# Performance work log

Hardware: AMD Instinct MI355X
Metric: run time of the kernel (lower is better)

The kernel has to match this reference:

```python
import jax, jax.numpy as jnp
import numpy as np

NUM_ANCHORS_LIST = [6400, 1600, 400]  # 640x640 input, strides 8/16/32
STRIDES = [8, 16, 32]
GRID_SIZES = [80, 40, 20]
TOPK = 9
EPS = 1e-9


def _make_anchor_bboxes():
    boxes = []
    for stride, size in zip(STRIDES, GRID_SIZES):
        c = (np.arange(size, dtype=np.float32) + 0.5) * stride
        cx, cy = np.meshgrid(c, c)
        half = stride / 2.0
        b = np.stack([cx - half, cy - half, cx + half, cy + half], axis=-1)
        boxes.append(b.reshape(-1, 4))
    return jnp.asarray(np.concatenate(boxes, axis=0))  # [8400,4]


def _random_boxes(key, shape_prefix, img=640.0):
    k1, k2 = jax.random.split(key)
    cxy = jax.random.uniform(k1, shape_prefix + (2,), minval=0.0, maxval=img)
    wh = jax.random.uniform(k2, shape_prefix + (2,), minval=8.0, maxval=160.0)
    x1y1 = jnp.clip(cxy - wh / 2, 0.0, img)
    x2y2 = jnp.clip(cxy + wh / 2, 0.0, img)
    return jnp.concatenate([x1y1, x2y2], axis=-1).astype(jnp.float32)


def setup_inputs() -> dict:
    key = jax.random.key(0)
    kg, kp, kl, km = jax.random.split(key, 4)
    B, N, M, C = 16, 8400, 128, 80
    return {
        "anchor_bboxes": _make_anchor_bboxes(),               # [N,4]
        "gt_labels": jax.random.randint(kl, (B, M, 1), 0, C).astype(jnp.int64),
        "gt_bboxes": _random_boxes(kg, (B, M)),               # [B,M,4]
        "mask_gt": jax.random.randint(km, (B, M, 1), 0, 2).astype(jnp.int32),
        "pred_bboxes": _random_boxes(kp, (B, N)),             # [B,N,4]
        "num_classes": C,
    }


def _batch_bbox_iou(box1, box2):
    # box1 [B,N,4], box2 [B,M,4] -> [B,N,M]
    area1 = (box1[..., 2] - box1[..., 0]) * (box1[..., 3] - box1[..., 1])
    area2 = (box2[..., 2] - box2[..., 0]) * (box2[..., 3] - box2[..., 1])
    ix1 = jnp.maximum(box1[:, :, None, 0], box2[:, None, :, 0])
    iy1 = jnp.maximum(box1[:, :, None, 1], box2[:, None, :, 1])
    ix2 = jnp.minimum(box1[:, :, None, 2], box2[:, None, :, 2])
    iy2 = jnp.minimum(box1[:, :, None, 3], box2[:, None, :, 3])
    inter = jnp.maximum(ix2 - ix1, 0.0) * jnp.maximum(iy2 - iy1, 0.0)
    union = area1[:, :, None] + area2[:, None, :] - inter
    return inter / (union + EPS)


def reference(anchor_bboxes, gt_labels, gt_bboxes, mask_gt, pred_bboxes, num_classes):
    B, M = gt_bboxes.shape[0], gt_bboxes.shape[1]
    N = anchor_bboxes.shape[0]
    labels = gt_labels[..., 0].astype(jnp.int32)           # [B,M]

    ac = (anchor_bboxes[:, :2] + anchor_bboxes[:, 2:]) / 2  # [N,2]
    gc = (gt_bboxes[..., :2] + gt_bboxes[..., 2:]) / 2      # [B,M,2]
    # cdist via expanded quadratic form (avoids [B,N,M,2] intermediate)
    a2 = jnp.sum(ac * ac, axis=-1)                          # [N]
    g2 = jnp.sum(gc * gc, axis=-1)                          # [B,M]
    d2 = a2[None, :, None] + g2[:, None, :] - 2.0 * jnp.einsum('nc,bmc->bnm', ac, gc)
    distances = jnp.sqrt(jnp.maximum(d2, 0.0))              # [B,N,M]

    # per-level topk closest anchors per GT -> candidate mask [B,N,M]
    bidx = jnp.arange(B)[:, None, None]
    midx = jnp.arange(M)[None, :, None]
    level_masks = []
    start = 0
    for ln in NUM_ANCHORS_LIST:
        ld = distances[:, start:start + ln, :]               # [B,ln,M]
        k = min(TOPK, ln)
        _, idx = jax.lax.top_k(-jnp.swapaxes(ld, 1, 2), k)   # [B,M,k] anchor idx
        lm = jnp.zeros((B, ln, M), dtype=bool).at[bidx, idx, midx].set(True)
        level_masks.append(lm)
        start += ln
    candidate_mask = jnp.concatenate(level_masks, axis=1)    # [B,N,M]

    ious = _batch_bbox_iou(jnp.broadcast_to(anchor_bboxes[None], (B, N, 4)), gt_bboxes)
    cm_f = candidate_mask.astype(ious.dtype)
    cand_ious = ious * cm_f
    count = jnp.maximum(cm_f.sum(axis=1), 1.0)               # [B,M]
    mean = cand_ious.sum(axis=1) / count
    sq_mean = jnp.sum(cand_ious * cand_ious, axis=1) / count # mask is 0/1
    std = jnp.sqrt(jnp.maximum(sq_mean - mean * mean, 0.0))
    thr = mean + std                                         # [B,M]

    is_pos = candidate_mask & (ious >= thr[:, None, :])
    center_in_gt = ((ac[None, :, None, 0] >= gt_bboxes[:, None, :, 0])
                    & (ac[None, :, None, 0] <= gt_bboxes[:, None, :, 2])
                    & (ac[None, :, None, 1] >= gt_bboxes[:, None, :, 1])
                    & (ac[None, :, None, 1] <= gt_bboxes[:, None, :, 3]))
    is_pos = is_pos & center_in_gt & (mask_gt[..., 0] > 0)[:, None, :]

    fg_mask = jnp.any(is_pos, axis=-1)                       # [B,N]
    pos_ious = jnp.where(is_pos, ious, 0.0)
    max_gt_idx = jnp.argmax(pos_ious, axis=-1)               # [B,N]

    fg_f = fg_mask.astype(ious.dtype)
    assigned_labels = jnp.take_along_axis(labels, max_gt_idx, axis=1) * fg_mask.astype(jnp.int32)
    assigned_bboxes = jnp.take_along_axis(gt_bboxes, max_gt_idx[..., None], axis=1) * fg_f[..., None]
    assigned_ious = jnp.take_along_axis(ious, max_gt_idx[..., None], axis=2)[..., 0] * fg_f

    pred_ious = _batch_bbox_iou(pred_bboxes, gt_bboxes)
    pred_assigned = jnp.take_along_axis(pred_ious, max_gt_idx[..., None], axis=2)[..., 0] * fg_f
    assigned_ious = assigned_ious * pred_assigned

    assigned_scores = jax.nn.one_hot(assigned_labels, num_classes, dtype=ious.dtype) \
        * (assigned_ious * fg_f)[..., None]                  # [B,N,C]
    return assigned_labels, assigned_bboxes, assigned_scores, fg_mask
```

## Files before the change

kernel.cpp:

```cpp
#include <hip/hip_runtime.h>
#include <stdint.h>

#define B_ 16
#define N_ 8400
#define M_ 128

__device__ __forceinline__ float iou_box(float ax1, float ay1, float ax2, float ay2,
                                         float bx1, float by1, float bx2, float by2) {
    float area1 = __fmul_rn(__fsub_rn(ax2, ax1), __fsub_rn(ay2, ay1));
    float area2 = __fmul_rn(__fsub_rn(bx2, bx1), __fsub_rn(by2, by1));
    float ix1 = fmaxf(ax1, bx1), iy1 = fmaxf(ay1, by1);
    float ix2 = fminf(ax2, bx2), iy2 = fminf(ay2, by2);
    float iw = fmaxf(__fsub_rn(ix2, ix1), 0.0f);
    float ih = fmaxf(__fsub_rn(iy2, iy1), 0.0f);
    float inter = __fmul_rn(iw, ih);
    float uni = __fsub_rn(__fadd_rn(area1, area2), inter);
    return __fdiv_rn(inter, __fadd_rn(uni, 1e-9f));
}

__global__ __launch_bounds__(128) void assign_kernel(
    const float* __restrict__ gt_bboxes,
    const int* __restrict__ mask_gt,
    unsigned long long* __restrict__ ws) {
    const int tid = threadIdx.x;
    const int r = tid >> 5;
    const int s = tid & 31;
    const int g = blockIdx.x * 32 + s;
    const int b = g >> 7;
    const int m = g & (M_ - 1);
    const bool active = (mask_gt[g] != 0);

    __shared__ int   s_idx[27 * 32];
    __shared__ float s_iou[27 * 32];
    __shared__ int   s_cin[27 * 32];
    __shared__ float s_thr[32];

    const float* gp = gt_bboxes + (size_t)g * 4;
    const float gx1 = gp[0], gy1 = gp[1], gx2 = gp[2], gy2 = gp[3];
    const float gcx = __fmul_rn(__fadd_rn(gx1, gx2), 0.5f);
    const float gcy = __fmul_rn(__fadd_rn(gy1, gy2), 0.5f);
    const float g2 = __fadd_rn(__fmul_rn(gcx, gcx), __fmul_rn(gcy, gcy));

    if (r < 3 && active) {
        const int   size  = (r == 0) ? 80 : ((r == 1) ? 40 : 20);
        const int   start = (r == 0) ? 0 : ((r == 1) ? 6400 : 8000);
        const float st    = (r == 0) ? 8.0f : ((r == 1) ? 16.0f : 32.0f);
        const float inv   = (r == 0) ? 0.125f : ((r == 1) ? 0.0625f : 0.03125f);

        int jl = (int)floorf(gcx * inv - 0.5f) - 2;
        int il = (int)floorf(gcy * inv - 0.5f) - 2;
        jl = min(max(jl, 0), size - 6);
        il = min(max(il, 0), size - 6);

        unsigned long long tk[9];
#pragma unroll
        for (int k = 0; k < 9; ++k) tk[k] = ~0ULL;

        for (int wy = 0; wy < 6; ++wy) {
            const int   i   = il + wy;
            const float acy = __fmul_rn(__fadd_rn((float)i, 0.5f), st);
            for (int wx = 0; wx < 6; ++wx) {
                const int   j   = jl + wx;
                const float acx = __fmul_rn(__fadd_rn((float)j, 0.5f), st);
                const int   n   = start + i * size + j;
                float a2  = __fadd_rn(__fmul_rn(acx, acx), __fmul_rn(acy, acy));
                float dot = __fadd_rn(__fmul_rn(acx, gcx), __fmul_rn(acy, gcy));
                float d2  = __fsub_rn(__fadd_rn(a2, g2), __fmul_rn(2.0f, dot));
                float dist = __fsqrt_rn(fmaxf(d2, 0.0f));
                unsigned long long key =
                    ((unsigned long long)__float_as_uint(dist) << 32) | (unsigned)n;
                if (key < tk[8]) tk[8] = key;
#pragma unroll
                for (int q = 8; q >= 1; --q) {
                    unsigned long long lo = tk[q - 1] < tk[q] ? tk[q - 1] : tk[q];
                    unsigned long long hi = tk[q - 1] < tk[q] ? tk[q] : tk[q - 1];
                    tk[q - 1] = lo;
                    tk[q] = hi;
                }
            }
        }

        int v[9];
#pragma unroll
        for (int k = 0; k < 9; ++k) v[k] = (int)(tk[k] & 0xFFFFFFFFu);
#pragma unroll
        for (int rr = 0; rr < 9; ++rr) {
#pragma unroll
            for (int p = (rr & 1); p + 1 < 9; p += 2) {
                int lo = min(v[p], v[p + 1]);
                int hi = max(v[p], v[p + 1]);
                v[p] = lo; v[p + 1] = hi;
            }
        }
#pragma unroll
        for (int k = 0; k < 9; ++k) s_idx[(r * 9 + k) * 32 + s] = v[k];
    }
    __syncthreads();

#pragma unroll
    for (int q = 0; q < 7; ++q) {
        const int kk = r + 4 * q;
        if (kk < 27 && active) {
            const int   l     = kk / 9;
            const int   size  = (l == 0) ? 80 : ((l == 1) ? 40 : 20);
            const int   start = (l == 0) ? 0 : ((l == 1) ? 6400 : 8000);
            const float st    = (l == 0) ? 8.0f : ((l == 1) ? 16.0f : 32.0f);
            const float half  = __fmul_rn(st, 0.5f);
            const int n = s_idx[kk * 32 + s];
            const int loc = n - start;
            const int i = loc / size;
            const int j = loc - i * size;
            float acx = __fmul_rn(__fadd_rn((float)j, 0.5f), st);
            float acy = __fmul_rn(__fadd_rn((float)i, 0.5f), st);
            float ax1 = __fsub_rn(acx, half), ay1 = __fsub_rn(acy, half);
            float ax2 = __fadd_rn(acx, half), ay2 = __fadd_rn(acy, half);
            float iou = iou_box(ax1, ay1, ax2, ay2, gx1, gy1, gx2, gy2);
            s_iou[kk * 32 + s] = iou;
            s_cin[kk * 32 + s] =
                (acx >= gx1 && acx <= gx2 && acy >= gy1 && acy <= gy2) ? 1 : 0;
        }
    }
    __syncthreads();

    if (r == 0 && active) {
        float tot = 0.0f, tot2 = 0.0f;
#pragma unroll
        for (int kk = 0; kk < 27; ++kk) {
            const float iou = s_iou[kk * 32 + s];
            tot  = __fadd_rn(tot, iou);
            tot2 = __fadd_rn(tot2, __fmul_rn(iou, iou));
        }
        float mean = __fdiv_rn(tot, 27.0f);
        float sqm  = __fdiv_rn(tot2, 27.0f);
        float var  = __fsub_rn(sqm, __fmul_rn(mean, mean));
        float stdv = __fsqrt_rn(fmaxf(var, 0.0f));
        s_thr[s] = __fadd_rn(mean, stdv);
    }
    __syncthreads();

    if (active) {
        const float thr = s_thr[s];
#pragma unroll
        for (int q = 0; q < 7; ++q) {
            const int kk = r + 4 * q;
            if (kk < 27) {
                const float iou = s_iou[kk * 32 + s];
                if (s_cin[kk * 32 + s] && iou >= thr) {
                    unsigned long long packed =
                        ((unsigned long long)(0xC0000000u | __float_as_uint(iou)) << 32) |
                        (unsigned long long)(0xFFFFFFFFu - (unsigned)m);
                    atomicMax(&ws[(size_t)b * N_ + s_idx[kk * 32 + s]], packed);
                }
            }
        }
    }
}

__global__ __launch_bounds__(256) void finalize_kernel(
    const int* __restrict__ gt_labels,
    const float* __restrict__ gt_bboxes,
    const float* __restrict__ pred_bboxes,
    const int* __restrict__ num_classes_p,
    const unsigned long long* __restrict__ ws,
    float* __restrict__ out) {
    const int idx = blockIdx.x * 256 + threadIdx.x;
    const int C = num_classes_p[0];

    float4* sp = (float4*)(out + (size_t)B_ * N_ * 5) + (size_t)blockIdx.x * 5120;
    const float4 z4 = make_float4(0.f, 0.f, 0.f, 0.f);
    for (int k = threadIdx.x; k < 5120; k += 256) sp[k] = z4;
    __syncthreads();

    if (idx >= B_ * N_) return;
    const int b = idx / N_;

    const unsigned long long w = ws[idx];
    const bool fg = (w >> 62) == 3ULL;
    float labelf = 0.0f;
    float4 bb = make_float4(0.f, 0.f, 0.f, 0.f);
    float v = 0.0f, fgf = 0.0f;
    int label = 0;
    if (fg) {
        fgf = 1.0f;
        const unsigned mm = 0xFFFFFFFFu - (unsigned)(w & 0xFFFFFFFFu);
        const float a_iou = __uint_as_float((unsigned)((w >> 32) & 0x3FFFFFFFu));
        label = gt_labels[b * M_ + (int)mm];
        labelf = (float)label;
        const float* gg = gt_bboxes + ((size_t)b * M_ + mm) * 4;
        bb.x = gg[0]; bb.y = gg[1]; bb.z = gg[2]; bb.w = gg[3];
        const float* p = pred_bboxes + (size_t)idx * 4;
        float piou = iou_box(p[0], p[1], p[2], p[3], bb.x, bb.y, bb.z, bb.w);
        v = __fmul_rn(a_iou, piou);
    }

    out[idx] = labelf;
    ((float4*)(out + (size_t)B_ * N_))[idx] = bb;
    if (fg) out[(size_t)B_ * N_ * 5 + (size_t)idx * C + label] = v;
    out[(size_t)B_ * N_ * (5 + C) + idx] = fgf;
}

extern "C" void kernel_launch(void* const* d_in, const int* in_sizes, int n_in,
                              void* d_out, int out_size, void* d_ws, size_t ws_size,
                              hipStream_t stream) {
    const int*   gt_labels  = (const int*)d_in[1];
    const float* gt_bboxes  = (const float*)d_in[2];
    const int*   mask_gt    = (const int*)d_in[3];
    const float* pred       = (const float*)d_in[4];
    const int*   ncls       = (const int*)d_in[5];
    unsigned long long* ws  = (unsigned long long*)d_ws;
    float* out              = (float*)d_out;

    assign_kernel<<<64, 128, 0, stream>>>(gt_bboxes, mask_gt, ws);
    finalize_kernel<<<(B_ * N_ + 255) / 256, 256, 0, stream>>>(
        gt_labels, gt_bboxes, pred, ncls, ws, out);
}
```

Measured before the change: 89.52 us.

## Fuse assignment and finalize into one kernel with per-tile shared-memory winners

Merges the two kernels into one grid over (anchor tile, batch). Each block recomputes the top-k candidates, IoU thresholds and center tests for all 128 GTs of its batch, then resolves winners with shared-memory atomics restricted to its 256-anchor tile. It then writes the outputs, including a coalesced float4 write of the score tensor in one pass instead of zeroing it and scattering into it. This removes the global workspace, its global atomics and the second launch, at the cost of redundant candidate computation in every block (33x per batch).

```diff
diff --git a/kernel.cpp b/kernel.cpp
--- a/kernel.cpp
+++ b/kernel.cpp
@@ -18,95 +18,120 @@
     return __fdiv_rn(inter, __fadd_rn(uni, 1e-9f));
 }
 
-__global__ __launch_bounds__(128) void assign_kernel(
+__global__ __launch_bounds__(256) void fused_kernel(
+    const int* __restrict__ gt_labels,
     const float* __restrict__ gt_bboxes,
     const int* __restrict__ mask_gt,
-    unsigned long long* __restrict__ ws) {
-    const int tid = threadIdx.x;
-    const int r = tid >> 5;
-    const int s = tid & 31;
-    const int g = blockIdx.x * 32 + s;
-    const int b = g >> 7;
-    const int m = g & (M_ - 1);
-    const bool active = (mask_gt[g] != 0);
-
-    __shared__ int   s_idx[27 * 32];
-    __shared__ float s_iou[27 * 32];
-    __shared__ int   s_cin[27 * 32];
-    __shared__ float s_thr[32];
-
-    const float* gp = gt_bboxes + (size_t)g * 4;
-    const float gx1 = gp[0], gy1 = gp[1], gx2 = gp[2], gy2 = gp[3];
-    const float gcx = __fmul_rn(__fadd_rn(gx1, gx2), 0.5f);
-    const float gcy = __fmul_rn(__fadd_rn(gy1, gy2), 0.5f);
-    const float g2 = __fadd_rn(__fmul_rn(gcx, gcx), __fmul_rn(gcy, gcy));
-
-    if (r < 3 && active) {
-        const int   size  = (r == 0) ? 80 : ((r == 1) ? 40 : 20);
-        const int   start = (r == 0) ? 0 : ((r == 1) ? 6400 : 8000);
-        const float st    = (r == 0) ? 8.0f : ((r == 1) ? 16.0f : 32.0f);
-        const float inv   = (r == 0) ? 0.125f : ((r == 1) ? 0.0625f : 0.03125f);
-
-        int jl = (int)floorf(gcx * inv - 0.5f) - 2;
-        int il = (int)floorf(gcy * inv - 0.5f) - 2;
-        jl = min(max(jl, 0), size - 6);
-        il = min(max(il, 0), size - 6);
-
-        unsigned long long tk[9];
-#pragma unroll
-        for (int k = 0; k < 9; ++k) tk[k] = ~0ULL;
-
-        for (int wy = 0; wy < 6; ++wy) {
-            const int   i   = il + wy;
-            const float acy = __fmul_rn(__fadd_rn((float)i, 0.5f), st);
-            for (int wx = 0; wx < 6; ++wx) {
-                const int   j   = jl + wx;
-                const float acx = __fmul_rn(__fadd_rn((float)j, 0.5f), st);
-                const int   n   = start + i * size + j;
-                float a2  = __fadd_rn(__fmul_rn(acx, acx), __fmul_rn(acy, acy));
-                float dot = __fadd_rn(__fmul_rn(acx, gcx), __fmul_rn(acy, gcy));
-                float d2  = __fsub_rn(__fadd_rn(a2, g2), __fmul_rn(2.0f, dot));
-                float dist = __fsqrt_rn(fmaxf(d2, 0.0f));
-                unsigned long long key =
-                    ((unsigned long long)__float_as_uint(dist) << 32) | (unsigned)n;
-                if (key < tk[8]) tk[8] = key;
-#pragma unroll
-                for (int q = 8; q >= 1; --q) {
-                    unsigned long long lo = tk[q - 1] < tk[q] ? tk[q - 1] : tk[q];
-                    unsigned long long hi = tk[q - 1] < tk[q] ? tk[q] : tk[q - 1];
-                    tk[q - 1] = lo;
-                    tk[q] = hi;
+    const float* __restrict__ pred_bboxes,
+    const int* __restrict__ num_classes_p,
+    float* __restrict__ out) {
+    const int tile = blockIdx.x;
+    const int b    = blockIdx.y;
+    const int t    = threadIdx.x;
+    const int C    = num_classes_p[0];
+
+    __shared__ float s_gx1[M_], s_gy1[M_], s_gx2[M_], s_gy2[M_];
+    __shared__ float s_gcx[M_], s_gcy[M_], s_g2[M_], s_thr[M_];
+    __shared__ int   s_mask[M_], s_lab[M_];
+    __shared__ int   s_cand[27 * M_];
+    __shared__ float s_ciou[27 * M_];
+    __shared__ unsigned s_ccin[M_];
+    __shared__ unsigned long long s_win[256];
+    __shared__ int   s_slab[256];
+    __shared__ float s_sv[256];
+    __shared__ int   s_sfg[256];
+
+    s_win[t] = 0ULL;
+    if (t < M_) {
+        const int gi = b * M_ + t;
+        const float4 gb = ((const float4*)gt_bboxes)[gi];
+        s_gx1[t] = gb.x; s_gy1[t] = gb.y; s_gx2[t] = gb.z; s_gy2[t] = gb.w;
+        const float gcx = __fmul_rn(__fadd_rn(gb.x, gb.z), 0.5f);
+        const float gcy = __fmul_rn(__fadd_rn(gb.y, gb.w), 0.5f);
+        s_gcx[t] = gcx; s_gcy[t] = gcy;
+        s_g2[t]  = __fadd_rn(__fmul_rn(gcx, gcx), __fmul_rn(gcy, gcy));
+        s_mask[t] = mask_gt[gi];
+        s_lab[t]  = gt_labels[gi];
+    }
+    __syncthreads();
+
+#pragma unroll
+    for (int rep = 0; rep < 2; ++rep) {
+        const int T = t + rep * 256;
+        if (T < 384) {
+            const int l = T >> 7;
+            const int m = T & (M_ - 1);
+            if (s_mask[m]) {
+                const int   size  = (l == 0) ? 80 : ((l == 1) ? 40 : 20);
+                const int   start = (l == 0) ? 0 : ((l == 1) ? 6400 : 8000);
+                const float st    = (l == 0) ? 8.0f : ((l == 1) ? 16.0f : 32.0f);
+                const float inv   = (l == 0) ? 0.125f : ((l == 1) ? 0.0625f : 0.03125f);
+                const float gcx = s_gcx[m], gcy = s_gcy[m], g2 = s_g2[m];
+
+                int jl = (int)floorf(gcx * inv - 0.5f) - 2;
+                int il = (int)floorf(gcy * inv - 0.5f) - 2;
+                jl = min(max(jl, 0), size - 6);
+                il = min(max(il, 0), size - 6);
+
+                unsigned long long tk[9];
+#pragma unroll
+                for (int k = 0; k < 9; ++k) tk[k] = ~0ULL;
+
+                for (int wy = 0; wy < 6; ++wy) {
+                    const int   i   = il + wy;
+                    const float acy = __fmul_rn(__fadd_rn((float)i, 0.5f), st);
+                    for (int wx = 0; wx < 6; ++wx) {
+                        const int   j   = jl + wx;
+                        const float acx = __fmul_rn(__fadd_rn((float)j, 0.5f), st);
+                        const int   n   = start + i * size + j;
+                        float a2  = __fadd_rn(__fmul_rn(acx, acx), __fmul_rn(acy, acy));
+                        float dot = __fadd_rn(__fmul_rn(acx, gcx), __fmul_rn(acy, gcy));
+                        float d2  = __fsub_rn(__fadd_rn(a2, g2), __fmul_rn(2.0f, dot));
+                        float dist = __fsqrt_rn(fmaxf(d2, 0.0f));
+                        unsigned long long key =
+                            ((unsigned long long)__float_as_uint(dist) << 32) | (unsigned)n;
+                        if (key < tk[8]) tk[8] = key;
+#pragma unroll
+                        for (int q = 8; q >= 1; --q) {
+                            unsigned long long lo = tk[q - 1] < tk[q] ? tk[q - 1] : tk[q];
+                            unsigned long long hi = tk[q - 1] < tk[q] ? tk[q] : tk[q - 1];
+                            tk[q - 1] = lo;
+                            tk[q] = hi;
+                        }
+                    }
                 }
+
+                int v[9];
+#pragma unroll
+                for (int k = 0; k < 9; ++k) v[k] = (int)(tk[k] & 0xFFFFFFFFu);
+#pragma unroll
+                for (int rr = 0; rr < 9; ++rr) {
+#pragma unroll
+                    for (int p = (rr & 1); p + 1 < 9; p += 2) {
+                        int lo = min(v[p], v[p + 1]);
+                        int hi = max(v[p], v[p + 1]);
+                        v[p] = lo; v[p + 1] = hi;
+                    }
+                }
+#pragma unroll
+                for (int k = 0; k < 9; ++k) s_cand[(l * 9 + k) * M_ + m] = v[k];
             }
         }
-
-        int v[9];
-#pragma unroll
-        for (int k = 0; k < 9; ++k) v[k] = (int)(tk[k] & 0xFFFFFFFFu);
-#pragma unroll
-        for (int rr = 0; rr < 9; ++rr) {
-#pragma unroll
-            for (int p = (rr & 1); p + 1 < 9; p += 2) {
-                int lo = min(v[p], v[p + 1]);
-                int hi = max(v[p], v[p + 1]);
-                v[p] = lo; v[p + 1] = hi;
-            }
-        }
-#pragma unroll
-        for (int k = 0; k < 9; ++k) s_idx[(r * 9 + k) * 32 + s] = v[k];
-    }
-    __syncthreads();
-
-#pragma unroll
-    for (int q = 0; q < 7; ++q) {
-        const int kk = r + 4 * q;
-        if (kk < 27 && active) {
+    }
+    __syncthreads();
+
+    if (t < M_ && s_mask[t]) {
+        const float gx1 = s_gx1[t], gy1 = s_gy1[t], gx2 = s_gx2[t], gy2 = s_gy2[t];
+        unsigned cin = 0;
+        float tot = 0.0f, tot2 = 0.0f;
+#pragma unroll
+        for (int kk = 0; kk < 27; ++kk) {
             const int   l     = kk / 9;
             const int   size  = (l == 0) ? 80 : ((l == 1) ? 40 : 20);
             const int   start = (l == 0) ? 0 : ((l == 1) ? 6400 : 8000);
             const float st    = (l == 0) ? 8.0f : ((l == 1) ? 16.0f : 32.0f);
             const float half  = __fmul_rn(st, 0.5f);
-            const int n = s_idx[kk * 32 + s];
+            const int n = s_cand[kk * M_ + t];
             const int loc = n - start;
             const int i = loc / size;
             const int j = loc - i * size;
@@ -115,88 +140,85 @@
             float ax1 = __fsub_rn(acx, half), ay1 = __fsub_rn(acy, half);
             float ax2 = __fadd_rn(acx, half), ay2 = __fadd_rn(acy, half);
             float iou = iou_box(ax1, ay1, ax2, ay2, gx1, gy1, gx2, gy2);
-            s_iou[kk * 32 + s] = iou;
-            s_cin[kk * 32 + s] =
-                (acx >= gx1 && acx <= gx2 && acy >= gy1 && acy <= gy2) ? 1 : 0;
-        }
-    }
-    __syncthreads();
-
-    if (r == 0 && active) {
-        float tot = 0.0f, tot2 = 0.0f;
-#pragma unroll
-        for (int kk = 0; kk < 27; ++kk) {
-            const float iou = s_iou[kk * 32 + s];
+            s_ciou[kk * M_ + t] = iou;
+            if (acx >= gx1 && acx <= gx2 && acy >= gy1 && acy <= gy2)
+                cin |= (1u << kk);
             tot  = __fadd_rn(tot, iou);
             tot2 = __fadd_rn(tot2, __fmul_rn(iou, iou));
         }
+        s_ccin[t] = cin;
         float mean = __fdiv_rn(tot, 27.0f);
         float sqm  = __fdiv_rn(tot2, 27.0f);
         float var  = __fsub_rn(sqm, __fmul_rn(mean, mean));
         float stdv = __fsqrt_rn(fmaxf(var, 0.0f));
-        s_thr[s] = __fadd_rn(mean, stdv);
-    }
-    __syncthreads();
-
-    if (active) {
-        const float thr = s_thr[s];
-#pragma unroll
-        for (int q = 0; q < 7; ++q) {
-            const int kk = r + 4 * q;
-            if (kk < 27) {
-                const float iou = s_iou[kk * 32 + s];
-                if (s_cin[kk * 32 + s] && iou >= thr) {
-                    unsigned long long packed =
-                        ((unsigned long long)(0xC0000000u | __float_as_uint(iou)) << 32) |
-                        (unsigned long long)(0xFFFFFFFFu - (unsigned)m);
-                    atomicMax(&ws[(size_t)b * N_ + s_idx[kk * 32 + s]], packed);
-                }
+        s_thr[t] = __fadd_rn(mean, stdv);
+    }
+    __syncthreads();
+
+    for (int T = t; T < M_ * 27; T += 256) {
+        const int m  = T / 27;
+        const int kk = T - m * 27;
+        if (!s_mask[m]) continue;
+        const float iou = s_ciou[kk * M_ + m];
+        if (((s_ccin[m] >> kk) & 1u) && iou >= s_thr[m]) {
+            const int n = s_cand[kk * M_ + m];
+            const int slot = n - tile * 256;
+            if (slot >= 0 && slot < 256) {
+                unsigned long long packed =
+                    ((unsigned long long)__float_as_uint(iou) << 32) |
+                    (unsigned long long)(0xFFFFFFFFu - (unsigned)m);
+                atomicMax(&s_win[slot], packed);
             }
         }
     }
-}
-
-__global__ __launch_bounds__(256) void finalize_kernel(
-    const int* __restrict__ gt_labels,
-    const float* __restrict__ gt_bboxes,
-    const float* __restrict__ pred_bboxes,
-    const int* __restrict__ num_classes_p,
-    const unsigned long long* __restrict__ ws,
-    float* __restrict__ out) {
-    const int idx = blockIdx.x * 256 + threadIdx.x;
-    const int C = num_classes_p[0];
-
-    float4* sp = (float4*)(out + (size_t)B_ * N_ * 5) + (size_t)blockIdx.x * 5120;
-    const float4 z4 = make_float4(0.f, 0.f, 0.f, 0.f);
-    for (int k = threadIdx.x; k < 5120; k += 256) sp[k] = z4;
-    __syncthreads();
-
-    if (idx >= B_ * N_) return;
-    const int b = idx / N_;
-
-    const unsigned long long w = ws[idx];
-    const bool fg = (w >> 62) == 3ULL;
-    float labelf = 0.0f;
-    float4 bb = make_float4(0.f, 0.f, 0.f, 0.f);
-    float v = 0.0f, fgf = 0.0f;
-    int label = 0;
-    if (fg) {
-        fgf = 1.0f;
-        const unsigned mm = 0xFFFFFFFFu - (unsigned)(w & 0xFFFFFFFFu);
-        const float a_iou = __uint_as_float((unsigned)((w >> 32) & 0x3FFFFFFFu));
-        label = gt_labels[b * M_ + (int)mm];
-        labelf = (float)label;
-        const float* gg = gt_bboxes + ((size_t)b * M_ + mm) * 4;
-        bb.x = gg[0]; bb.y = gg[1]; bb.z = gg[2]; bb.w = gg[3];
-        const float* p = pred_bboxes + (size_t)idx * 4;
-        float piou = iou_box(p[0], p[1], p[2], p[3], bb.x, bb.y, bb.z, bb.w);
-        v = __fmul_rn(a_iou, piou);
-    }
-
-    out[idx] = labelf;
-    ((float4*)(out + (size_t)B_ * N_))[idx] = bb;
-    if (fg) out[(size_t)B_ * N_ * 5 + (size_t)idx * C + label] = v;
-    out[(size_t)B_ * N_ * (5 + C) + idx] = fgf;
+    __syncthreads();
+
+    const int n = tile * 256 + t;
+    int   lab = 0, fg = 0;
+    float v_out = 0.0f;
+    if (n < N_) {
+        const unsigned long long w = s_win[t];
+        float labelf = 0.0f;
+        float4 bb = make_float4(0.f, 0.f, 0.f, 0.f);
+        float fgf = 0.0f;
+        if (w != 0ULL) {
+            fg = 1; fgf = 1.0f;
+            const unsigned mm = 0xFFFFFFFFu - (unsigned)(w & 0xFFFFFFFFu);
+            const float a_iou = __uint_as_float((unsigned)(w >> 32));
+            lab = s_lab[mm];
+            labelf = (float)lab;
+            bb.x = s_gx1[mm]; bb.y = s_gy1[mm];
+            bb.z = s_gx2[mm]; bb.w = s_gy2[mm];
+            const float4 p = ((const float4*)pred_bboxes)[(size_t)b * N_ + n];
+            float piou = iou_box(p.x, p.y, p.z, p.w, bb.x, bb.y, bb.z, bb.w);
+            v_out = __fmul_rn(a_iou, piou);
+        }
+        const size_t idxG = (size_t)b * N_ + n;
+        out[idxG] = labelf;
+        ((float4*)(out + (size_t)B_ * N_))[idxG] = bb;
+        out[(size_t)B_ * N_ * (5 + C) + idxG] = fgf;
+    }
+    s_slab[t] = lab;
+    s_sv[t]   = v_out;
+    s_sfg[t]  = fg;
+    __syncthreads();
+
+    const int cnt = min(256, N_ - tile * 256);
+    const int c4  = C >> 2;
+    const int total4 = cnt * c4;
+    float4* sc = (float4*)(out + (size_t)B_ * N_ * 5) +
+                 ((size_t)b * N_ + (size_t)tile * 256) * c4;
+    for (int f = t; f < total4; f += 256) {
+        const int a = f / c4;
+        const int q = f - a * c4;
+        float4 z = make_float4(0.f, 0.f, 0.f, 0.f);
+        if (s_sfg[a]) {
+            const int c0 = q << 2;
+            const int La = s_slab[a];
+            if (La >= c0 && La < c0 + 4) ((float*)&z)[La - c0] = s_sv[a];
+        }
+        sc[f] = z;
+    }
 }
 
 extern "C" void kernel_launch(void* const* d_in, const int* in_sizes, int n_in,
@@ -207,10 +229,10 @@
     const int*   mask_gt    = (const int*)d_in[3];
     const float* pred       = (const float*)d_in[4];
     const int*   ncls       = (const int*)d_in[5];
-    unsigned long long* ws  = (unsigned long long*)d_ws;
     float* out              = (float*)d_out;
-
-    assign_kernel<<<64, 128, 0, stream>>>(gt_bboxes, mask_gt, ws);
-    finalize_kernel<<<(B_ * N_ + 255) / 256, 256, 0, stream>>>(
-        gt_labels, gt_bboxes, pred, ncls, ws, out);
+    (void)d_ws; (void)ws_size;
+
+    dim3 grid((N_ + 255) / 256, B_);
+    fused_kernel<<<grid, 256, 0, stream>>>(gt_labels, gt_bboxes, mask_gt,
+                                           pred, ncls, out);
 }
```

New measurement: 115.6 us. 29.2% more time.

## Parallelize per-GT top-k with wave bitonic sort and fuse score-row writes

Applied to the files above, without the earlier changes.

The assign kernel now uses one block per ground-truth box instead of 32 boxes per block. Each 64-lane wave handles one pyramid level and replaces the serial 36-element insertion top-k with a wave-wide bitonic sort over shuffles. This spreads the work over 2048 blocks instead of 64 and cuts per-thread serial latency. In finalize, the separate zero-fill followed by a scattered score write becomes a single pass of float4 stores that places each anchor's score inline. That removes one write pass and a barrier, but assumes C is divisible by 4 and that B*N is a multiple of 256.

```diff
diff --git a/kernel.cpp b/kernel.cpp
--- a/kernel.cpp
+++ b/kernel.cpp
@@ -18,71 +18,74 @@
     return __fdiv_rn(inter, __fadd_rn(uni, 1e-9f));
 }
 
-__global__ __launch_bounds__(128) void assign_kernel(
+__global__ __launch_bounds__(192) void assign_kernel(
     const float* __restrict__ gt_bboxes,
     const int* __restrict__ mask_gt,
     unsigned long long* __restrict__ ws) {
-    const int tid = threadIdx.x;
-    const int r = tid >> 5;
-    const int s = tid & 31;
-    const int g = blockIdx.x * 32 + s;
+    const int g = blockIdx.x;
+    if (mask_gt[g] == 0) return;
     const int b = g >> 7;
     const int m = g & (M_ - 1);
-    const bool active = (mask_gt[g] != 0);
-
-    __shared__ int   s_idx[27 * 32];
-    __shared__ float s_iou[27 * 32];
-    __shared__ int   s_cin[27 * 32];
-    __shared__ float s_thr[32];
-
-    const float* gp = gt_bboxes + (size_t)g * 4;
-    const float gx1 = gp[0], gy1 = gp[1], gx2 = gp[2], gy2 = gp[3];
+    const int t = threadIdx.x;
+    const int w = t >> 6;
+    const int lane = t & 63;
+
+    __shared__ int   s_idx[27];
+    __shared__ float s_iou[27];
+    __shared__ int   s_cin[27];
+    __shared__ float s_thr;
+
+    const float4 gb = ((const float4*)gt_bboxes)[g];
+    const float gx1 = gb.x, gy1 = gb.y, gx2 = gb.z, gy2 = gb.w;
     const float gcx = __fmul_rn(__fadd_rn(gx1, gx2), 0.5f);
     const float gcy = __fmul_rn(__fadd_rn(gy1, gy2), 0.5f);
     const float g2 = __fadd_rn(__fmul_rn(gcx, gcx), __fmul_rn(gcy, gcy));
 
-    if (r < 3 && active) {
-        const int   size  = (r == 0) ? 80 : ((r == 1) ? 40 : 20);
-        const int   start = (r == 0) ? 0 : ((r == 1) ? 6400 : 8000);
-        const float st    = (r == 0) ? 8.0f : ((r == 1) ? 16.0f : 32.0f);
-        const float inv   = (r == 0) ? 0.125f : ((r == 1) ? 0.0625f : 0.03125f);
-
-        int jl = (int)floorf(gcx * inv - 0.5f) - 2;
-        int il = (int)floorf(gcy * inv - 0.5f) - 2;
-        jl = min(max(jl, 0), size - 6);
-        il = min(max(il, 0), size - 6);
-
-        unsigned long long tk[9];
-#pragma unroll
-        for (int k = 0; k < 9; ++k) tk[k] = ~0ULL;
-
-        for (int wy = 0; wy < 6; ++wy) {
-            const int   i   = il + wy;
-            const float acy = __fmul_rn(__fadd_rn((float)i, 0.5f), st);
-            for (int wx = 0; wx < 6; ++wx) {
-                const int   j   = jl + wx;
-                const float acx = __fmul_rn(__fadd_rn((float)j, 0.5f), st);
-                const int   n   = start + i * size + j;
-                float a2  = __fadd_rn(__fmul_rn(acx, acx), __fmul_rn(acy, acy));
-                float dot = __fadd_rn(__fmul_rn(acx, gcx), __fmul_rn(acy, gcy));
-                float d2  = __fsub_rn(__fadd_rn(a2, g2), __fmul_rn(2.0f, dot));
-                float dist = __fsqrt_rn(fmaxf(d2, 0.0f));
-                unsigned long long key =
-                    ((unsigned long long)__float_as_uint(dist) << 32) | (unsigned)n;
-                if (key < tk[8]) tk[8] = key;
-#pragma unroll
-                for (int q = 8; q >= 1; --q) {
-                    unsigned long long lo = tk[q - 1] < tk[q] ? tk[q - 1] : tk[q];
-                    unsigned long long hi = tk[q - 1] < tk[q] ? tk[q] : tk[q - 1];
-                    tk[q - 1] = lo;
-                    tk[q] = hi;
-                }
-            }
-        }
-
+    const int   size  = (w == 0) ? 80 : ((w == 1) ? 40 : 20);
+    const int   start = (w == 0) ? 0 : ((w == 1) ? 6400 : 8000);
+    const float st    = (w == 0) ? 8.0f : ((w == 1) ? 16.0f : 32.0f);
+    const float inv   = (w == 0) ? 0.125f : ((w == 1) ? 0.0625f : 0.03125f);
+
+    int jl = (int)floorf(gcx * inv - 0.5f) - 2;
+    int il = (int)floorf(gcy * inv - 0.5f) - 2;
+    jl = min(max(jl, 0), size - 6);
+    il = min(max(il, 0), size - 6);
+
+    unsigned long long key = ~0ULL;
+    if (lane < 36) {
+        const int wy = lane / 6;
+        const int wx = lane - wy * 6;
+        const int   i   = il + wy;
+        const int   j   = jl + wx;
+        const float acy = __fmul_rn(__fadd_rn((float)i, 0.5f), st);
+        const float acx = __fmul_rn(__fadd_rn((float)j, 0.5f), st);
+        const int   n   = start + i * size + j;
+        float a2  = __fadd_rn(__fmul_rn(acx, acx), __fmul_rn(acy, acy));
+        float dot = __fadd_rn(__fmul_rn(acx, gcx), __fmul_rn(acy, gcy));
+        float d2  = __fsub_rn(__fadd_rn(a2, g2), __fmul_rn(2.0f, dot));
+        float dist = __fsqrt_rn(fmaxf(d2, 0.0f));
+        key = ((unsigned long long)__float_as_uint(dist) << 32) | (unsigned)n;
+    }
+
+#pragma unroll
+    for (int k = 2; k <= 64; k <<= 1) {
+#pragma unroll
+        for (int j = k >> 1; j > 0; j >>= 1) {
+            unsigned long long other = __shfl_xor(key, j, 64);
+            const bool up = ((lane & k) == 0);
+            const bool keepMin = (((lane & j) == 0) == up);
+            const unsigned long long mn = key < other ? key : other;
+            const unsigned long long mx = key < other ? other : key;
+            key = keepMin ? mn : mx;
+        }
+    }
+    if (lane < 9) s_idx[w * 9 + lane] = (int)(key & 0xFFFFFFFFu);
+    __syncthreads();
+
+    if (t < 3) {
         int v[9];
 #pragma unroll
-        for (int k = 0; k < 9; ++k) v[k] = (int)(tk[k] & 0xFFFFFFFFu);
+        for (int k = 0; k < 9; ++k) v[k] = s_idx[t * 9 + k];
 #pragma unroll
         for (int rr = 0; rr < 9; ++rr) {
 #pragma unroll
@@ -93,40 +96,35 @@
             }
         }
 #pragma unroll
-        for (int k = 0; k < 9; ++k) s_idx[(r * 9 + k) * 32 + s] = v[k];
-    }
-    __syncthreads();
-
-#pragma unroll
-    for (int q = 0; q < 7; ++q) {
-        const int kk = r + 4 * q;
-        if (kk < 27 && active) {
-            const int   l     = kk / 9;
-            const int   size  = (l == 0) ? 80 : ((l == 1) ? 40 : 20);
-            const int   start = (l == 0) ? 0 : ((l == 1) ? 6400 : 8000);
-            const float st    = (l == 0) ? 8.0f : ((l == 1) ? 16.0f : 32.0f);
-            const float half  = __fmul_rn(st, 0.5f);
-            const int n = s_idx[kk * 32 + s];
-            const int loc = n - start;
-            const int i = loc / size;
-            const int j = loc - i * size;
-            float acx = __fmul_rn(__fadd_rn((float)j, 0.5f), st);
-            float acy = __fmul_rn(__fadd_rn((float)i, 0.5f), st);
-            float ax1 = __fsub_rn(acx, half), ay1 = __fsub_rn(acy, half);
-            float ax2 = __fadd_rn(acx, half), ay2 = __fadd_rn(acy, half);
-            float iou = iou_box(ax1, ay1, ax2, ay2, gx1, gy1, gx2, gy2);
-            s_iou[kk * 32 + s] = iou;
-            s_cin[kk * 32 + s] =
-                (acx >= gx1 && acx <= gx2 && acy >= gy1 && acy <= gy2) ? 1 : 0;
-        }
-    }
-    __syncthreads();
-
-    if (r == 0 && active) {
+        for (int k = 0; k < 9; ++k) s_idx[t * 9 + k] = v[k];
+    }
+    __syncthreads();
+
+    if (t < 27) {
+        const int   l      = t / 9;
+        const int   size2  = (l == 0) ? 80 : ((l == 1) ? 40 : 20);
+        const int   start2 = (l == 0) ? 0 : ((l == 1) ? 6400 : 8000);
+        const float st2    = (l == 0) ? 8.0f : ((l == 1) ? 16.0f : 32.0f);
+        const float half   = __fmul_rn(st2, 0.5f);
+        const int n = s_idx[t];
+        const int loc = n - start2;
+        const int i = loc / size2;
+        const int j = loc - i * size2;
+        float acx = __fmul_rn(__fadd_rn((float)j, 0.5f), st2);
+        float acy = __fmul_rn(__fadd_rn((float)i, 0.5f), st2);
+        float ax1 = __fsub_rn(acx, half), ay1 = __fsub_rn(acy, half);
+        float ax2 = __fadd_rn(acx, half), ay2 = __fadd_rn(acy, half);
+        float iou = iou_box(ax1, ay1, ax2, ay2, gx1, gy1, gx2, gy2);
+        s_iou[t] = iou;
+        s_cin[t] = (acx >= gx1 && acx <= gx2 && acy >= gy1 && acy <= gy2) ? 1 : 0;
+    }
+    __syncthreads();
+
+    if (t == 0) {
         float tot = 0.0f, tot2 = 0.0f;
 #pragma unroll
         for (int kk = 0; kk < 27; ++kk) {
-            const float iou = s_iou[kk * 32 + s];
+            const float iou = s_iou[kk];
             tot  = __fadd_rn(tot, iou);
             tot2 = __fadd_rn(tot2, __fmul_rn(iou, iou));
         }
@@ -134,24 +132,17 @@
         float sqm  = __fdiv_rn(tot2, 27.0f);
         float var  = __fsub_rn(sqm, __fmul_rn(mean, mean));
         float stdv = __fsqrt_rn(fmaxf(var, 0.0f));
-        s_thr[s] = __fadd_rn(mean, stdv);
-    }
-    __syncthreads();
-
-    if (active) {
-        const float thr = s_thr[s];
-#pragma unroll
-        for (int q = 0; q < 7; ++q) {
-            const int kk = r + 4 * q;
-            if (kk < 27) {
-                const float iou = s_iou[kk * 32 + s];
-                if (s_cin[kk * 32 + s] && iou >= thr) {
-                    unsigned long long packed =
-                        ((unsigned long long)(0xC0000000u | __float_as_uint(iou)) << 32) |
-                        (unsigned long long)(0xFFFFFFFFu - (unsigned)m);
-                    atomicMax(&ws[(size_t)b * N_ + s_idx[kk * 32 + s]], packed);
-                }
-            }
+        s_thr = __fadd_rn(mean, stdv);
+    }
+    __syncthreads();
+
+    if (t < 27) {
+        const float iou = s_iou[t];
+        if (s_cin[t] && iou >= s_thr) {
+            unsigned long long packed =
+                ((unsigned long long)(0xC0000000u | __float_as_uint(iou)) << 32) |
+                (unsigned long long)(0xFFFFFFFFu - (unsigned)m);
+            atomicMax(&ws[(size_t)b * N_ + s_idx[t]], packed);
         }
     }
 }
@@ -163,16 +154,14 @@
     const int* __restrict__ num_classes_p,
     const unsigned long long* __restrict__ ws,
     float* __restrict__ out) {
-    const int idx = blockIdx.x * 256 + threadIdx.x;
+    const int t = threadIdx.x;
+    const int idx = blockIdx.x * 256 + t;
+    const int b = idx / N_;
     const int C = num_classes_p[0];
 
-    float4* sp = (float4*)(out + (size_t)B_ * N_ * 5) + (size_t)blockIdx.x * 5120;
-    const float4 z4 = make_float4(0.f, 0.f, 0.f, 0.f);
-    for (int k = threadIdx.x; k < 5120; k += 256) sp[k] = z4;
-    __syncthreads();
-
-    if (idx >= B_ * N_) return;
-    const int b = idx / N_;
+    __shared__ int   s_slab[256];
+    __shared__ float s_sv[256];
+    __shared__ int   s_sfg[256];
 
     const unsigned long long w = ws[idx];
     const bool fg = (w >> 62) == 3ULL;
@@ -195,8 +184,27 @@
 
     out[idx] = labelf;
     ((float4*)(out + (size_t)B_ * N_))[idx] = bb;
-    if (fg) out[(size_t)B_ * N_ * 5 + (size_t)idx * C + label] = v;
     out[(size_t)B_ * N_ * (5 + C) + idx] = fgf;
+
+    s_slab[t] = label;
+    s_sv[t]   = v;
+    s_sfg[t]  = fg ? 1 : 0;
+    __syncthreads();
+
+    const int c4 = C >> 2;
+    const int total4 = 256 * c4;
+    float4* sc = (float4*)(out + (size_t)B_ * N_ * 5) + (size_t)blockIdx.x * 256 * c4;
+    for (int f = t; f < total4; f += 256) {
+        const int a = f / c4;
+        const int q = f - a * c4;
+        float4 z = make_float4(0.f, 0.f, 0.f, 0.f);
+        if (s_sfg[a]) {
+            const int c0 = q << 2;
+            const int La = s_slab[a];
+            if (La >= c0 && La < c0 + 4) ((float*)&z)[La - c0] = s_sv[a];
+        }
+        sc[f] = z;
+    }
 }
 
 extern "C" void kernel_launch(void* const* d_in, const int* in_sizes, int n_in,
@@ -210,7 +218,7 @@
     unsigned long long* ws  = (unsigned long long*)d_ws;
     float* out              = (float*)d_out;
 
-    assign_kernel<<<64, 128, 0, stream>>>(gt_bboxes, mask_gt, ws);
-    finalize_kernel<<<(B_ * N_ + 255) / 256, 256, 0, stream>>>(
+    assign_kernel<<<B_ * M_, 192, 0, stream>>>(gt_bboxes, mask_gt, ws);
+    finalize_kernel<<<(B_ * N_) / 256, 256, 0, stream>>>(
         gt_labels, gt_bboxes, pred, ncls, ws, out);
 }
```

Measured after the change: 99.38 us. +11.0%, slower.
